# Kernel tuning notes

Hardware: AMD Instinct MI355X
Metric: run time of the kernel (lower is better)

## Reference

```python
import jax, jax.numpy as jnp
import numpy as np

N_SRC = 100_000
N_DST = 100_000
N_EDGES = 1_600_000
D_IN = 256
N_HEADS = 4
OUT_FEATS = 32
NEG_SLOPE = 0.2


def setup_inputs() -> dict:
    key = jax.random.key(0)
    k1, k2, k3, k4, k5, k6, k7 = jax.random.split(key, 7)
    return {
        "feat_src": jax.random.normal(k1, (N_SRC, D_IN), dtype=jnp.float32),
        "feat_dst": jax.random.normal(k2, (N_DST, D_IN), dtype=jnp.float32),
        "w_src": jax.random.normal(k3, (D_IN, N_HEADS * OUT_FEATS), dtype=jnp.float32) * 0.05,
        "w_dst": jax.random.normal(k4, (D_IN, N_HEADS * OUT_FEATS), dtype=jnp.float32) * 0.05,
        "attn": jax.random.normal(k5, (N_HEADS, 2 * OUT_FEATS), dtype=jnp.float32) * 0.05,
        "src_idx": jax.random.randint(k6, (N_EDGES,), 0, N_SRC, dtype=jnp.int32),
        "dst_idx": jax.random.randint(k7, (N_EDGES,), 0, N_DST, dtype=jnp.int32),
    }


def reference(feat_src, feat_dst, w_src, w_dst, attn, src_idx, dst_idx):
    H, two_d = attn.shape
    D = two_d // 2
    n_dst = feat_dst.shape[0]
    # node transformations (dropout rate = 0.0 -> identity)
    fs = (feat_src @ w_src).reshape(-1, H, D)   # [Ns, H, D]
    fd = (feat_dst @ w_dst).reshape(-1, H, D)   # [Nd, H, D]
    # per-node attention logits: e_dst uses first half, e_src second half
    e_dst = (fd * attn[:, :D]).sum(-1)          # [Nd, H]
    e_src = (fs * attn[:, D:]).sum(-1)          # [Ns, H]
    # u_add_v on edges + leaky relu
    e = e_src[src_idx] + e_dst[dst_idx]         # [E, H]
    e = jnp.where(e > 0, e, NEG_SLOPE * e)
    # edge softmax: segment softmax over incoming edges of each dst node
    m = jax.ops.segment_max(e, dst_idx, num_segments=n_dst)       # [Nd, H]
    m = jnp.where(jnp.isfinite(m), m, 0.0)                        # empty segments
    ex = jnp.exp(e - m[dst_idx])                                  # [E, H]
    denom = jax.ops.segment_sum(ex, dst_idx, num_segments=n_dst)  # [Nd, H]
    a = ex / denom[dst_idx]                                       # [E, H]
    # u_mul_e + sum aggregation
    msg = fs[src_idx] * a[:, :, None]                             # [E, H, D]
    out = jax.ops.segment_sum(msg, dst_idx, num_segments=n_dst)   # [Nd, H, D]
    return jax.nn.relu(out.reshape(n_dst, H * D))
```

## Files before the change

### kernel.cpp

```cpp
#include <hip/hip_runtime.h>

#define N_NODES 100000
#define N_EDGES 1600000
#define D_IN    256
#define HD      128
#define NEG_SLOPE 0.2f

#define BUK_SH    5
#define BUK_NODES 32
#define NBUCKETS ((N_NODES + BUK_NODES - 1) / BUK_NODES)
#define BUK_CAP  1024
#define BUK_CH   8192
#define NB_BUK   ((N_EDGES + BUK_CH - 1) / BUK_CH)
#define NB_PREP 33

#define NTILES  (N_NODES / 16)
#define NB_CAST 2048
#define NB_EDSTB 512
#define GEMM_ROWS 128
#define NB_GEMM ((N_NODES + GEMM_ROWS - 1) / GEMM_ROWS)

#define EX_STRIDE 1032

typedef __bf16 bf16x8 __attribute__((ext_vector_type(8)));
typedef float  f32x4  __attribute__((ext_vector_type(4)));

__device__ __forceinline__ float lrelu_exp(float v) {
  v = v > 0.f ? v : NEG_SLOPE * v;
  return __expf(v);
}
__device__ __forceinline__ float bf_lo(unsigned u) { return __uint_as_float(u << 16); }
__device__ __forceinline__ float bf_hi(unsigned u) { return __uint_as_float(u & 0xffff0000u); }
__device__ __forceinline__ unsigned pk2(float a, float b) {
  __bf16 ba = (__bf16)a, bb = (__bf16)b;
  return ((unsigned)*(const ushort*)&bb << 16) | *(const ushort*)&ba;
}

__global__ __launch_bounds__(1024) void prep_bucket_kernel(const float* __restrict__ w_src,
                                                           const float* __restrict__ w_dst,
                                                           const float* __restrict__ attn,
                                                           ushort* __restrict__ wT,
                                                           float* __restrict__ v_dst,
                                                           const int* __restrict__ src,
                                                           const int* __restrict__ dstv,
                                                           int* __restrict__ bcur,
                                                           unsigned* __restrict__ ebuk) {
  const int bid = blockIdx.x;
  const int tid = threadIdx.x;
  if (bid < 32) {
    int idx = bid * 1024 + tid;
    int k = idx >> 7, n = idx & 127;
    __bf16 bv = (__bf16)w_src[idx];
    wT[n * 256 + k] = *(const ushort*)&bv;
  } else if (bid == 32) {
    if (tid < 256) {
      int k = tid;
      for (int h = 0; h < 4; ++h) {
        float s = 0.f;
        for (int d = 0; d < 32; ++d)
          s += w_dst[k * HD + h * 32 + d] * attn[h * 64 + d];
        v_dst[k * 4 + h] = s;
      }
    }
  } else {
    __shared__ int bh[NBUCKETS];
    const int e0 = (bid - NB_PREP) * BUK_CH;
    for (int j = tid; j < NBUCKETS; j += 1024) bh[j] = 0;
    __syncthreads();
    for (int i = tid; i < BUK_CH; i += 1024) {
      int e = e0 + i;
      if (e < N_EDGES) atomicAdd(&bh[dstv[e] >> BUK_SH], 1);
    }
    __syncthreads();
    for (int j = tid; j < NBUCKETS; j += 1024) {
      int c = bh[j];
      bh[j] = (c > 0) ? atomicAdd(&bcur[j], c) : 0;
    }
    __syncthreads();
    for (int i = tid; i < BUK_CH; i += 1024) {
      int e = e0 + i;
      if (e < N_EDGES) {
        int d = dstv[e];
        int b = d >> BUK_SH;
        int p = atomicAdd(&bh[b], 1);
        if (p < BUK_CAP)
          ebuk[(size_t)b * BUK_CAP + p] =
              ((unsigned)src[e] << BUK_SH) | (unsigned)(d & (BUK_NODES - 1));
      }
    }
  }
}

__global__ __launch_bounds__(512) void cast_edst_kernel(const float* __restrict__ feat_src,
                                                        ushort* __restrict__ As,
                                                        const float* __restrict__ feat_dst,
                                                        const float* __restrict__ v_dst,
                                                        float* __restrict__ e_dst) {
  __shared__ float4 vds[256];
  const int bid = blockIdx.x;
  const int tid = threadIdx.x;
  if (bid < NB_CAST) {
    const int rl = tid >> 5;
    const int j  = tid & 31;
    const int dst_off = (j >> 2) * 64 + (j & 3) * 16 + rl;
    uint4* Ap = (uint4*)As;
    for (int t = bid; t < NTILES; t += NB_CAST) {
      const float* sp = feat_src + ((size_t)t * 16 + rl) * D_IN + j * 8;
      float4 f0 = *(const float4*)sp;
      float4 f1 = *(const float4*)(sp + 4);
      uint4 pk;
      pk.x = pk2(f0.x, f0.y); pk.y = pk2(f0.z, f0.w);
      pk.z = pk2(f1.x, f1.y); pk.w = pk2(f1.z, f1.w);
      Ap[(size_t)t * 512 + dst_off] = pk;
    }
  } else {
    if (tid < 256) vds[tid] = ((const float4*)v_dst)[tid];
    __syncthreads();
    const int l = tid & 15;
    const int grp = tid >> 4;
    for (int n = (bid - NB_CAST) * 32 + grp; n < N_NODES; n += NB_EDSTB * 32) {
      const float* fp = feat_dst + (size_t)n * D_IN;
      float ax = 0.f, ay = 0.f, az = 0.f, aw = 0.f;
#pragma unroll
      for (int c = 0; c < 4; ++c) {
        const int k0 = c * 64 + l * 4;
        float4 f = *(const float4*)(fp + k0);
        float4 v0 = vds[k0 + 0], v1 = vds[k0 + 1], v2 = vds[k0 + 2], v3 = vds[k0 + 3];
        ax = fmaf(f.x, v0.x, fmaf(f.y, v1.x, fmaf(f.z, v2.x, fmaf(f.w, v3.x, ax))));
        ay = fmaf(f.x, v0.y, fmaf(f.y, v1.y, fmaf(f.z, v2.y, fmaf(f.w, v3.y, ay))));
        az = fmaf(f.x, v0.z, fmaf(f.y, v1.z, fmaf(f.z, v2.z, fmaf(f.w, v3.z, az))));
        aw = fmaf(f.x, v0.w, fmaf(f.y, v1.w, fmaf(f.z, v2.w, fmaf(f.w, v3.w, aw))));
      }
#pragma unroll
      for (int off = 1; off < 16; off <<= 1) {
        ax += __shfl_xor(ax, off, 64);
        ay += __shfl_xor(ay, off, 64);
        az += __shfl_xor(az, off, 64);
        aw += __shfl_xor(aw, off, 64);
      }
      if (l == 0) *(float4*)(e_dst + (size_t)n * 4) = make_float4(ax, ay, az, aw);
    }
  }
}

__global__ __launch_bounds__(512, 4) void gemm_kernel(const ushort* __restrict__ As,
                                                      const ushort* __restrict__ wT16,
                                                      const float* __restrict__ attn,
                                                      unsigned* __restrict__ fs16,
                                                      float* __restrict__ e_src,
                                                      int M) {
  __shared__ ushort Bl[128 * 256];
  const int bid = blockIdx.x;
  const int tid = threadIdx.x;
  const int lane = tid & 63, wid = tid >> 6;
  const int lr = lane & 15, hi = lane >> 4;

  {
    const uint4* wg4 = (const uint4*)wT16;
#pragma unroll
    for (int i = 0; i < 8; ++i) {
      int c = i * 512 + tid;
      int col = c >> 5;
      unsigned byte = ((unsigned)c * 16u) ^ (((unsigned)col & 31u) << 4);
      *(uint4*)((char*)Bl + byte) = wg4[c];
    }
  }

  int tile = bid * 8 + wid;
  if (tile >= NTILES) tile = NTILES - 1;
  const bf16x8* ap = (const bf16x8*)As + (size_t)tile * 512 + lane;

  bf16x8 afc = ap[0];

  f32x4 acc[8];
  const f32x4 zf = {0.f, 0.f, 0.f, 0.f};
#pragma unroll
  for (int n = 0; n < 8; ++n) acc[n] = zf;

  __syncthreads();

#pragma unroll
  for (int ks = 0; ks < 8; ++ks) {
    bf16x8 afn = afc;
    if (ks < 7) afn = ap[(ks + 1) * 64];
    bf16x8 bf[8];
#pragma unroll
    for (int n = 0; n < 8; ++n) {
      unsigned col = (unsigned)(n * 16 + lr);
      unsigned byte = (col * 512u + (unsigned)(ks * 64 + hi * 16)) ^ ((col & 31u) << 4);
      bf[n] = *(const bf16x8*)((const char*)Bl + byte);
    }
#pragma unroll
    for (int n = 0; n < 8; ++n)
      acc[n] = __builtin_amdgcn_mfma_f32_16x16x32_bf16(afc, bf[n], acc[n], 0, 0, 0);
    afc = afn;
  }

  const int bm = bid * GEMM_ROWS;

#pragma unroll
  for (int n = 0; n < 8; ++n) {
#pragma unroll
    for (int r4 = 0; r4 < 4; ++r4) {
      float val = acc[n][r4];
      float pv  = __shfl_xor(val, 1, 64);
      int gr = bm + wid * 16 + hi * 4 + r4;
      if (!(lane & 1) && gr < M) {
        __bf16 b0 = (__bf16)val, b1 = (__bf16)pv;
        unsigned pk = ((unsigned)*(const ushort*)&b1 << 16) | *(const ushort*)&b0;
        fs16[(size_t)gr * 64 + n * 8 + (lr >> 1)] = pk;
      }
    }
  }

#pragma unroll
  for (int gh = 0; gh < 4; ++gh) {
    float av0 = attn[gh * 64 + 32 + lr];
    float av1 = attn[gh * 64 + 48 + lr];
#pragma unroll
    for (int r4 = 0; r4 < 4; ++r4) {
      float s = acc[2 * gh][r4] * av0 + acc[2 * gh + 1][r4] * av1;
      s += __shfl_xor(s, 1, 64);
      s += __shfl_xor(s, 2, 64);
      s += __shfl_xor(s, 4, 64);
      s += __shfl_xor(s, 8, 64);
      int gr = bm + wid * 16 + hi * 4 + r4;
      if (lr == 0 && gr < M) e_src[(size_t)gr * 4 + gh] = s;
    }
  }
}

__global__ __launch_bounds__(256) void agg_kernel(const unsigned* __restrict__ ebuk,
                                                  const int* __restrict__ bcur,
                                                  const float4* __restrict__ e_src,
                                                  const float4* __restrict__ e_dst,
                                                  const unsigned* __restrict__ fs16,
                                                  float* __restrict__ out, int N) {
  __shared__ unsigned sorted_e[BUK_CAP];
  __shared__ float ex_s[4][EX_STRIDE];
  __shared__ int lcnt[BUK_NODES];
  __shared__ int lofs_s[BUK_NODES + 1];
  __shared__ int lcur[BUK_NODES];
  const int tid = threadIdx.x;
  const int wslot = tid >> 6;
  const int lane = tid & 63;
  const int lo = blockIdx.x * BUK_NODES;
  const size_t start = (size_t)blockIdx.x * BUK_CAP;
  const int cnt_e = min(bcur[blockIdx.x], BUK_CAP);

  if (tid < BUK_NODES) lcnt[tid] = 0;
  __syncthreads();
  for (int i = tid; i < cnt_e; i += 256)
    atomicAdd(&lcnt[ebuk[start + i] & (BUK_NODES - 1)], 1);
  __syncthreads();
  if (tid == 0) {
    int run = 0;
    for (int j = 0; j < BUK_NODES; ++j) {
      lofs_s[j] = run; lcur[j] = run; run += lcnt[j];
    }
    lofs_s[BUK_NODES] = run;
  }
  __syncthreads();
  for (int i = tid; i < cnt_e; i += 256) {
    unsigned e = ebuk[start + i];
    int p = atomicAdd(&lcur[e & (BUK_NODES - 1)], 1);
    sorted_e[p] = e;
  }
  __syncthreads();

  for (int i = tid; i < cnt_e; i += 256) {
    unsigned ent = sorted_e[i];
    int s  = (int)(ent >> BUK_SH);
    int dl = (int)(ent & (BUK_NODES - 1));
    float4 a  = e_src[s];
    float4 ed = e_dst[lo + dl];
    ex_s[0][i] = lrelu_exp(a.x + ed.x);
    ex_s[1][i] = lrelu_exp(a.y + ed.y);
    ex_s[2][i] = lrelu_exp(a.z + ed.z);
    ex_s[3][i] = lrelu_exp(a.w + ed.w);
  }
  __syncthreads();

  const int g = lane >> 4;
  const int q = lane & 15;
  const int h = q >> 2;

  for (int nl = wslot * 8; nl < wslot * 8 + 8; ++nl) {
    int node = lo + nl;
    if (node >= N) break;
    const int nb = lofs_s[nl], ne = lofs_s[nl + 1];
    float a0=0.f,a1=0.f,a2=0.f,a3=0.f,a4=0.f,a5=0.f,a6=0.f,a7=0.f,den=0.f;

    for (int cb = nb; cb < ne; cb += 16) {
      int e0 = cb + g, e1 = e0 + 4, e2 = e0 + 8, e3 = e0 + 12;
      bool p0 = e0 < ne, p1 = e1 < ne, p2 = e2 < ne, p3 = e3 < ne;
      int c0 = p0 ? e0 : nb, c1 = p1 ? e1 : nb, c2 = p2 ? e2 : nb, c3 = p3 ? e3 : nb;
      int s0 = (int)(sorted_e[c0] >> BUK_SH);
      int s1 = (int)(sorted_e[c1] >> BUK_SH);
      int s2 = (int)(sorted_e[c2] >> BUK_SH);
      int s3 = (int)(sorted_e[c3] >> BUK_SH);
      uint4 u0 = *(const uint4*)(fs16 + (size_t)s0 * 64 + q * 4);
      uint4 u1 = *(const uint4*)(fs16 + (size_t)s1 * 64 + q * 4);
      uint4 u2 = *(const uint4*)(fs16 + (size_t)s2 * 64 + q * 4);
      uint4 u3 = *(const uint4*)(fs16 + (size_t)s3 * 64 + q * 4);
      float x0 = p0 ? ex_s[h][c0] : 0.f;
      float x1 = p1 ? ex_s[h][c1] : 0.f;
      float x2 = p2 ? ex_s[h][c2] : 0.f;
      float x3 = p3 ? ex_s[h][c3] : 0.f;
      a0 = fmaf(x0, bf_lo(u0.x), a0); a1 = fmaf(x0, bf_hi(u0.x), a1);
      a2 = fmaf(x0, bf_lo(u0.y), a2); a3 = fmaf(x0, bf_hi(u0.y), a3);
      a4 = fmaf(x0, bf_lo(u0.z), a4); a5 = fmaf(x0, bf_hi(u0.z), a5);
      a6 = fmaf(x0, bf_lo(u0.w), a6); a7 = fmaf(x0, bf_hi(u0.w), a7);
      a0 = fmaf(x1, bf_lo(u1.x), a0); a1 = fmaf(x1, bf_hi(u1.x), a1);
      a2 = fmaf(x1, bf_lo(u1.y), a2); a3 = fmaf(x1, bf_hi(u1.y), a3);
      a4 = fmaf(x1, bf_lo(u1.z), a4); a5 = fmaf(x1, bf_hi(u1.z), a5);
      a6 = fmaf(x1, bf_lo(u1.w), a6); a7 = fmaf(x1, bf_hi(u1.w), a7);
      a0 = fmaf(x2, bf_lo(u2.x), a0); a1 = fmaf(x2, bf_hi(u2.x), a1);
      a2 = fmaf(x2, bf_lo(u2.y), a2); a3 = fmaf(x2, bf_hi(u2.y), a3);
      a4 = fmaf(x2, bf_lo(u2.z), a4); a5 = fmaf(x2, bf_hi(u2.z), a5);
      a6 = fmaf(x2, bf_lo(u2.w), a6); a7 = fmaf(x2, bf_hi(u2.w), a7);
      a0 = fmaf(x3, bf_lo(u3.x), a0); a1 = fmaf(x3, bf_hi(u3.x), a1);
      a2 = fmaf(x3, bf_lo(u3.y), a2); a3 = fmaf(x3, bf_hi(u3.y), a3);
      a4 = fmaf(x3, bf_lo(u3.z), a4); a5 = fmaf(x3, bf_hi(u3.z), a5);
      a6 = fmaf(x3, bf_lo(u3.w), a6); a7 = fmaf(x3, bf_hi(u3.w), a7);
      den += x0 + x1 + x2 + x3;
    }

    den += __shfl_xor(den, 16, 64); den += __shfl_xor(den, 32, 64);
    a0 += __shfl_xor(a0, 16, 64); a0 += __shfl_xor(a0, 32, 64);
    a1 += __shfl_xor(a1, 16, 64); a1 += __shfl_xor(a1, 32, 64);
    a2 += __shfl_xor(a2, 16, 64); a2 += __shfl_xor(a2, 32, 64);
    a3 += __shfl_xor(a3, 16, 64); a3 += __shfl_xor(a3, 32, 64);
    a4 += __shfl_xor(a4, 16, 64); a4 += __shfl_xor(a4, 32, 64);
    a5 += __shfl_xor(a5, 16, 64); a5 += __shfl_xor(a5, 32, 64);
    a6 += __shfl_xor(a6, 16, 64); a6 += __shfl_xor(a6, 32, 64);
    a7 += __shfl_xor(a7, 16, 64); a7 += __shfl_xor(a7, 32, 64);
    if (lane < 16) {
      float inv = den > 0.f ? 1.f / den : 0.f;
      float4 o1, o2;
      o1.x = fmaxf(a0 * inv, 0.f); o1.y = fmaxf(a1 * inv, 0.f);
      o1.z = fmaxf(a2 * inv, 0.f); o1.w = fmaxf(a3 * inv, 0.f);
      o2.x = fmaxf(a4 * inv, 0.f); o2.y = fmaxf(a5 * inv, 0.f);
      o2.z = fmaxf(a6 * inv, 0.f); o2.w = fmaxf(a7 * inv, 0.f);
      float* op = out + (size_t)node * HD + q * 8;
      *(float4*)(op)     = o1;
      *(float4*)(op + 4) = o2;
    }
  }
}

extern "C" void kernel_launch(void* const* d_in, const int* in_sizes, int n_in,
                              void* d_out, int out_size, void* d_ws, size_t ws_size,
                              hipStream_t stream) {
  const float* feat_src = (const float*)d_in[0];
  const float* feat_dst = (const float*)d_in[1];
  const float* w_src    = (const float*)d_in[2];
  const float* w_dst    = (const float*)d_in[3];
  const float* attn     = (const float*)d_in[4];
  const int*   src_idx  = (const int*)d_in[5];
  const int*   dst_idx  = (const int*)d_in[6];
  float* out = (float*)d_out;
  char* ws = (char*)d_ws;

  unsigned* fs16  = (unsigned*)(ws);
  float*    e_src = (float*)(ws + 25600000);
  float*    e_dst = (float*)(ws + 27200000);
  unsigned* ebuk  = (unsigned*)(ws + 28800000);
  float*    v_dst = (float*)(ws + 41600000);
  ushort*   wT16  = (ushort*)(ws + 41604096);
  int*      bcur  = (int*)  (ws + 41669632);

  ushort* As = (ushort*)d_out;

  hipMemsetAsync(bcur, 0, NBUCKETS * sizeof(int), stream);

  prep_bucket_kernel<<<NB_PREP + NB_BUK, 1024, 0, stream>>>(
      w_src, w_dst, attn, wT16, v_dst, src_idx, dst_idx, bcur, ebuk);

  cast_edst_kernel<<<NB_CAST + NB_EDSTB, 512, 0, stream>>>(
      feat_src, As, feat_dst, v_dst, e_dst);

  gemm_kernel<<<NB_GEMM, 512, 0, stream>>>(As, wT16, attn, fs16, e_src, N_NODES);

  agg_kernel<<<NBUCKETS, 256, 0, stream>>>(ebuk, bcur,
      (const float4*)e_src, (const float4*)e_dst, fs16, out, N_NODES);
}
```

Baseline: 194.2 us.

## Split cast and e_dst kernels and stage bf16 cast through LDS

The combined cast/e_dst kernel is split in two. The feat_src-to-bf16 cast becomes one block per 32-row group that loads the rows contiguously into shared memory, then writes the MFMA-tiled bf16 layout with contiguous 16-byte stores. The e_dst dot-product moves into its own 256-thread kernel launched after the GEMM, so it no longer competes with the cast for bandwidth. The aim is more coalesced global traffic in the cast; the cost is one extra kernel launch and an LDS round trip.

```diff
diff --git a/kernel.cpp b/kernel.cpp
--- a/kernel.cpp
+++ b/kernel.cpp
@@ -15,10 +15,10 @@
 #define NB_PREP 33
 
 #define NTILES  (N_NODES / 16)
-#define NB_CAST 2048
-#define NB_EDSTB 512
+#define NGROUPS (NTILES / 2)
 #define GEMM_ROWS 128
 #define NB_GEMM ((N_NODES + GEMM_ROWS - 1) / GEMM_ROWS)
+#define NB_EDST 1024
 
 #define EX_STRIDE 1032
 
@@ -91,55 +91,29 @@
   }
 }
 
-__global__ __launch_bounds__(512) void cast_edst_kernel(const float* __restrict__ feat_src,
-                                                        ushort* __restrict__ As,
-                                                        const float* __restrict__ feat_dst,
-                                                        const float* __restrict__ v_dst,
-                                                        float* __restrict__ e_dst) {
-  __shared__ float4 vds[256];
-  const int bid = blockIdx.x;
-  const int tid = threadIdx.x;
-  if (bid < NB_CAST) {
-    const int rl = tid >> 5;
-    const int j  = tid & 31;
-    const int dst_off = (j >> 2) * 64 + (j & 3) * 16 + rl;
-    uint4* Ap = (uint4*)As;
-    for (int t = bid; t < NTILES; t += NB_CAST) {
-      const float* sp = feat_src + ((size_t)t * 16 + rl) * D_IN + j * 8;
-      float4 f0 = *(const float4*)sp;
-      float4 f1 = *(const float4*)(sp + 4);
-      uint4 pk;
-      pk.x = pk2(f0.x, f0.y); pk.y = pk2(f0.z, f0.w);
-      pk.z = pk2(f1.x, f1.y); pk.w = pk2(f1.z, f1.w);
-      Ap[(size_t)t * 512 + dst_off] = pk;
-    }
-  } else {
-    if (tid < 256) vds[tid] = ((const float4*)v_dst)[tid];
-    __syncthreads();
-    const int l = tid & 15;
-    const int grp = tid >> 4;
-    for (int n = (bid - NB_CAST) * 32 + grp; n < N_NODES; n += NB_EDSTB * 32) {
-      const float* fp = feat_dst + (size_t)n * D_IN;
-      float ax = 0.f, ay = 0.f, az = 0.f, aw = 0.f;
-#pragma unroll
-      for (int c = 0; c < 4; ++c) {
-        const int k0 = c * 64 + l * 4;
-        float4 f = *(const float4*)(fp + k0);
-        float4 v0 = vds[k0 + 0], v1 = vds[k0 + 1], v2 = vds[k0 + 2], v3 = vds[k0 + 3];
-        ax = fmaf(f.x, v0.x, fmaf(f.y, v1.x, fmaf(f.z, v2.x, fmaf(f.w, v3.x, ax))));
-        ay = fmaf(f.x, v0.y, fmaf(f.y, v1.y, fmaf(f.z, v2.y, fmaf(f.w, v3.y, ay))));
-        az = fmaf(f.x, v0.z, fmaf(f.y, v1.z, fmaf(f.z, v2.z, fmaf(f.w, v3.z, az))));
-        aw = fmaf(f.x, v0.w, fmaf(f.y, v1.w, fmaf(f.z, v2.w, fmaf(f.w, v3.w, aw))));
-      }
-#pragma unroll
-      for (int off = 1; off < 16; off <<= 1) {
-        ax += __shfl_xor(ax, off, 64);
-        ay += __shfl_xor(ay, off, 64);
-        az += __shfl_xor(az, off, 64);
-        aw += __shfl_xor(aw, off, 64);
-      }
-      if (l == 0) *(float4*)(e_dst + (size_t)n * 4) = make_float4(ax, ay, az, aw);
-    }
+__global__ __launch_bounds__(512) void cast_kernel(const float* __restrict__ feat_src,
+                                                   ushort* __restrict__ As) {
+  __shared__ float Af[32][260];
+  const int tid = threadIdx.x;
+  const int g = blockIdx.x;
+  const float* sp = feat_src + (size_t)g * 8192;
+#pragma unroll
+  for (int k = 0; k < 4; ++k) {
+    int idx = k * 2048 + tid * 4;
+    float4 v = *(const float4*)(sp + idx);
+    *(float4*)&Af[idx >> 8][idx & 255] = v;
+  }
+  __syncthreads();
+  uint4* Ap = (uint4*)As + (size_t)g * 1024;
+#pragma unroll
+  for (int tl = 0; tl < 2; ++tl) {
+    const int s = tid;
+    const int rl = s & 15, hi = (s >> 4) & 3, ks = s >> 6;
+    const float* lp = &Af[tl * 16 + rl][ks * 32 + hi * 8];
+    uint4 pk;
+    pk.x = pk2(lp[0], lp[1]); pk.y = pk2(lp[2], lp[3]);
+    pk.z = pk2(lp[4], lp[5]); pk.w = pk2(lp[6], lp[7]);
+    Ap[tl * 512 + s] = pk;
   }
 }
 
@@ -227,6 +201,39 @@
       int gr = bm + wid * 16 + hi * 4 + r4;
       if (lr == 0 && gr < M) e_src[(size_t)gr * 4 + gh] = s;
     }
+  }
+}
+
+__global__ __launch_bounds__(256) void edst_kernel(const float* __restrict__ feat_dst,
+                                                   const float* __restrict__ v_dst,
+                                                   float* __restrict__ e_dst) {
+  __shared__ float4 vds[256];
+  const int tid = threadIdx.x;
+  vds[tid] = ((const float4*)v_dst)[tid];
+  __syncthreads();
+  const int l = tid & 15;
+  const int grp = tid >> 4;
+  for (int n = blockIdx.x * 16 + grp; n < N_NODES; n += NB_EDST * 16) {
+    const float* fp = feat_dst + (size_t)n * D_IN;
+    float ax = 0.f, ay = 0.f, az = 0.f, aw = 0.f;
+#pragma unroll
+    for (int c = 0; c < 4; ++c) {
+      const int k0 = c * 64 + l * 4;
+      float4 f = *(const float4*)(fp + k0);
+      float4 v0 = vds[k0 + 0], v1 = vds[k0 + 1], v2 = vds[k0 + 2], v3 = vds[k0 + 3];
+      ax = fmaf(f.x, v0.x, fmaf(f.y, v1.x, fmaf(f.z, v2.x, fmaf(f.w, v3.x, ax))));
+      ay = fmaf(f.x, v0.y, fmaf(f.y, v1.y, fmaf(f.z, v2.y, fmaf(f.w, v3.y, ay))));
+      az = fmaf(f.x, v0.z, fmaf(f.y, v1.z, fmaf(f.z, v2.z, fmaf(f.w, v3.z, az))));
+      aw = fmaf(f.x, v0.w, fmaf(f.y, v1.w, fmaf(f.z, v2.w, fmaf(f.w, v3.w, aw))));
+    }
+#pragma unroll
+    for (int off = 1; off < 16; off <<= 1) {
+      ax += __shfl_xor(ax, off, 64);
+      ay += __shfl_xor(ay, off, 64);
+      az += __shfl_xor(az, off, 64);
+      aw += __shfl_xor(aw, off, 64);
+    }
+    if (l == 0) *(float4*)(e_dst + (size_t)n * 4) = make_float4(ax, ay, az, aw);
   }
 }
 
@@ -377,10 +384,11 @@
   prep_bucket_kernel<<<NB_PREP + NB_BUK, 1024, 0, stream>>>(
       w_src, w_dst, attn, wT16, v_dst, src_idx, dst_idx, bcur, ebuk);
 
-  cast_edst_kernel<<<NB_CAST + NB_EDSTB, 512, 0, stream>>>(
-      feat_src, As, feat_dst, v_dst, e_dst);
+  cast_kernel<<<NGROUPS, 512, 0, stream>>>(feat_src, As);
 
   gemm_kernel<<<NB_GEMM, 512, 0, stream>>>(As, wT16, attn, fs16, e_src, N_NODES);
+
+  edst_kernel<<<NB_EDST, 256, 0, stream>>>(feat_dst, v_dst, e_dst);
 
   agg_kernel<<<NBUCKETS, 256, 0, stream>>>(ebuk, bcur,
       (const float4*)e_src, (const float4*)e_dst, fs16, out, N_NODES);
```

Result: faster. 185.8 us (-4.3%).
